# Kernel tuning notes

Hardware: AMD Instinct MI355X
Metric: run time of the kernel (lower is better)

Reference implementation:

```python
import jax, jax.numpy as jnp
import numpy as np

N, D_IN, D_H, D_OUT = 65536, 256, 256, 128
E, TOP_K = 16, 2


def setup_inputs() -> dict:
    key = jax.random.key(0)
    ks = jax.random.split(key, 16)
    s = 0.05
    inp = {
        'x': jax.random.normal(ks[0], (N, D_IN), jnp.float32),
        'W0': jax.random.normal(ks[1], (D_IN, D_H), jnp.float32) * s,
        'b0': jnp.zeros((D_H,), jnp.float32),
        'Wg1': jax.random.normal(ks[2], (D_H, E), jnp.float32) * s,
        'bg1': jnp.zeros((E,), jnp.float32),
        'We1': jax.random.normal(ks[3], (E, D_H, D_H), jnp.float32) * s,
        'be1': jnp.zeros((E, D_H), jnp.float32),
        'Wg2': jax.random.normal(ks[4], (D_H, E), jnp.float32) * s,
        'bg2': jnp.zeros((E,), jnp.float32),
        'We2': jax.random.normal(ks[5], (E, D_H, D_H), jnp.float32) * s,
        'be2': jnp.zeros((E, D_H), jnp.float32),
        'Wf': jax.random.normal(ks[6], (D_H, D_OUT), jnp.float32) * s,
        'bf': jnp.zeros((D_OUT,), jnp.float32),
    }
    return inp


def _moe_layer(h, Wg, bg, We, be):
    # naive gate: logits over experts, top-k, renormalized softmax of top-k vals
    logits = h @ Wg + bg                      # [N, E]
    gate_full = jax.nn.softmax(logits, axis=-1)  # returned 'gate' for std stat
    vals, idx = jax.lax.top_k(logits, TOP_K)  # [N, k]
    scores = jax.nn.softmax(vals, axis=-1)    # [N, k]
    # scatter top-k scores into dense combine weights [N, E]
    cw = (jax.nn.one_hot(idx, E, dtype=h.dtype) * scores[..., None]).sum(axis=1)
    # grouped GEMM expressed as masked per-expert GEMMs (E is small, fixed)
    y = jnp.zeros((h.shape[0], We.shape[-1]), h.dtype)
    for e in range(E):
        y = y + cw[:, e:e + 1] * (h @ We[e] + be[e])
    # torch.std defaults to unbiased (ddof=1)
    gate_std_mean = jnp.std(gate_full, axis=1, ddof=1).mean()
    return y, gate_std_mean


def reference(x, W0, b0, Wg1, bg1, We1, be1, Wg2, bg2, We2, be2, Wf, bf):
    h = jax.nn.relu(x @ W0 + b0)
    h, g1 = _moe_layer(h, Wg1, bg1, We1, be1)
    h = jax.nn.relu(h)
    h, g2 = _moe_layer(h, Wg2, bg2, We2, be2)
    h = jax.nn.relu(h)
    out = h @ Wf + bf
    gate_std_means_mean = (g1 + g2) * 0.5
    return out, gate_std_means_mean
```

## Files before the change

kernel.cpp:

```cpp
#include <hip/hip_runtime.h>
#include <math.h>

#define NT 65536
#define DH 256
#define DO 128
#define NE 16

struct RInfo { int e1, e2; float s1, s2; };

typedef __attribute__((ext_vector_type(8))) short bh8;
typedef __attribute__((ext_vector_type(4))) float fx4;

static __device__ __forceinline__ short f2bf(float f) {
    union { float f; unsigned u; } v; v.f = f;
    return (short)((v.u + 0x7FFFu + ((v.u >> 16) & 1u)) >> 16);
}

template<bool RELU>
__global__ __launch_bounds__(256)
void gemm_dense(const float* __restrict__ A, const float* __restrict__ B,
                const float* __restrict__ bias, float* __restrict__ C,
                int ncols)
{
    __shared__ float As[128][36];
    __shared__ float Bs[32][132];
    const int tid = threadIdx.x;
    const int tx = tid & 15, ty = tid >> 4;
    const int rowBase = blockIdx.x * 128;
    const int colBase = blockIdx.y * 128;

    float acc[8][8];
#pragma unroll
    for (int i = 0; i < 8; ++i)
#pragma unroll
        for (int j = 0; j < 8; ++j) acc[i][j] = 0.f;

    for (int kt = 0; kt < DH; kt += 32) {
        {
            const int r = tid >> 3, k4 = (tid & 7) << 2;
#pragma unroll
            for (int it = 0; it < 4; ++it) {
                const float4 v = *reinterpret_cast<const float4*>(
                    &A[(size_t)(rowBase + r + 32 * it) * DH + kt + k4]);
                *reinterpret_cast<float4*>(&As[r + 32 * it][k4]) = v;
            }
        }
        {
            const int kr = tid >> 5, c4 = (tid & 31) << 2;
#pragma unroll
            for (int it = 0; it < 4; ++it) {
                const float4 v = *reinterpret_cast<const float4*>(
                    &B[(size_t)(kt + kr + 8 * it) * ncols + colBase + c4]);
                *reinterpret_cast<float4*>(&Bs[kr + 8 * it][c4]) = v;
            }
        }
        __syncthreads();
#pragma unroll
        for (int k4 = 0; k4 < 32; k4 += 4) {
            alignas(16) float ar[8][4];
#pragma unroll
            for (int i = 0; i < 8; ++i)
                *reinterpret_cast<float4*>(ar[i]) =
                    *reinterpret_cast<const float4*>(&As[ty * 8 + i][k4]);
#pragma unroll
            for (int kk = 0; kk < 4; ++kk) {
                alignas(16) float br[8];
                *reinterpret_cast<float4*>(&br[0]) =
                    *reinterpret_cast<const float4*>(&Bs[k4 + kk][tx * 8]);
                *reinterpret_cast<float4*>(&br[4]) =
                    *reinterpret_cast<const float4*>(&Bs[k4 + kk][tx * 8 + 4]);
#pragma unroll
                for (int i = 0; i < 8; ++i) {
                    const float a = ar[i][kk];
#pragma unroll
                    for (int j = 0; j < 8; ++j)
                        acc[i][j] = fmaf(a, br[j], acc[i][j]);
                }
            }
        }
        __syncthreads();
    }
    alignas(16) float bb[8];
#pragma unroll
    for (int j = 0; j < 8; ++j) bb[j] = bias[colBase + tx * 8 + j];
#pragma unroll
    for (int i = 0; i < 8; ++i) {
        const size_t row = rowBase + ty * 8 + i;
        alignas(16) float o[8];
#pragma unroll
        for (int j = 0; j < 8; ++j) {
            float v = acc[i][j] + bb[j];
            if (RELU) v = fmaxf(v, 0.f);
            o[j] = v;
        }
        float* p = &C[row * (size_t)ncols + colBase + tx * 8];
        *reinterpret_cast<float4*>(p)     = *reinterpret_cast<float4*>(&o[0]);
        *reinterpret_cast<float4*>(p + 4) = *reinterpret_cast<float4*>(&o[4]);
    }
}

__global__ __launch_bounds__(256)
void gate_kernel(const float* __restrict__ H, const float* __restrict__ Wg,
                 const float* __restrict__ bg, RInfo* __restrict__ info,
                 float* gsum)
{
    __shared__ float wgs[256][17];
    __shared__ float hs[16][260];
    __shared__ float lg[16][17];
    __shared__ float sbg[16];
    __shared__ float sds[16];
    const int tid = threadIdx.x;
    const int rowBase = blockIdx.x * 16;

#pragma unroll
    for (int i = 0; i < 16; ++i) {
        const int idx = tid + 256 * i;
        wgs[idx >> 4][idx & 15] = Wg[idx];
    }
    if (tid < 16) sbg[tid] = bg[tid];
#pragma unroll
    for (int it = 0; it < 4; ++it) {
        const int flat = (tid + 256 * it) * 4;
        const int r = flat >> 8, k = flat & 255;
        *reinterpret_cast<float4*>(&hs[r][k]) =
            *reinterpret_cast<const float4*>(&H[(size_t)(rowBase + r) * DH + k]);
    }
    __syncthreads();
    {
        const int r = tid >> 4, e = tid & 15;
        float acc = 0.f;
#pragma unroll 8
        for (int k = 0; k < 256; ++k) acc = fmaf(hs[r][k], wgs[k][e], acc);
        lg[r][e] = acc + sbg[e];
    }
    __syncthreads();
    if (tid < 16) {
        const int row = rowBase + tid;
        float l[16];
#pragma unroll
        for (int i = 0; i < 16; ++i) l[i] = lg[tid][i];
        int i1 = 0; float v1 = l[0];
#pragma unroll
        for (int i = 1; i < 16; ++i) if (l[i] > v1) { v1 = l[i]; i1 = i; }
        int i2 = -1; float v2 = -INFINITY;
#pragma unroll
        for (int i = 0; i < 16; ++i) if (i != i1 && l[i] > v2) { v2 = l[i]; i2 = i; }
        const float t = expf(v2 - v1);
        const float s1 = 1.f / (1.f + t);
        const float s2 = t / (1.f + t);
        float p[16]; float S = 0.f;
#pragma unroll
        for (int i = 0; i < 16; ++i) { p[i] = expf(l[i] - v1); S += p[i]; }
        const float inv = 1.f / S;
        float sq = 0.f;
#pragma unroll
        for (int i = 0; i < 16; ++i) { const float q = p[i] * inv; sq = fmaf(q, q, sq); }
        const float var = (sq - 1.0f / 16.0f) * (1.0f / 15.0f);
        const float sd = sqrtf(fmaxf(var, 0.f));

        RInfo ri; ri.e1 = i1; ri.e2 = i2; ri.s1 = s1; ri.s2 = s2;
        info[row] = ri;
        sds[tid] = sd;
    }
    __syncthreads();
    if (tid == 0) {
        float s = 0.f;
#pragma unroll
        for (int i = 0; i < 16; ++i) s += sds[i];
        atomicAdd(gsum, s);
    }
}

__global__ void zero_gsum(float* gsum)
{
    if (threadIdx.x < 2) gsum[threadIdx.x] = 0.f;
}

__global__ __launch_bounds__(256)
void count_kernel(const RInfo* __restrict__ info, int* __restrict__ bc0,
                  int* __restrict__ bc1)
{
    __shared__ int h0[NE], h1[NE];
    const int tid = threadIdx.x, b = blockIdx.x;
    if (tid < NE) { h0[tid] = 0; h1[tid] = 0; }
    __syncthreads();
    const RInfo ri = info[b * 256 + tid];
    atomicAdd(&h0[ri.e1], 1);
    atomicAdd(&h1[ri.e2], 1);
    __syncthreads();
    if (tid < NE) {
        bc0[tid * 256 + b] = h0[tid];
        bc1[tid * 256 + b] = h1[tid];
    }
}

__global__ void scan2_kernel(const int* __restrict__ bc0, const int* __restrict__ bc1,
                             int* cnt0, int* cnt1, int* off0, int* off1,
                             int* __restrict__ bo0, int* __restrict__ bo1)
{
    __shared__ int tot0[NE], tot1[NE], base0[NE], base1[NE];
    const int t = threadIdx.x;
    if (t < NE) {
        int s = 0;
        for (int b = 0; b < 256; ++b) s += bc0[t * 256 + b];
        tot0[t] = s; cnt0[t] = s;
    } else if (t < 2 * NE) {
        const int e = t - NE;
        int s = 0;
        for (int b = 0; b < 256; ++b) s += bc1[e * 256 + b];
        tot1[e] = s; cnt1[e] = s;
    }
    __syncthreads();
    if (t == 0) { int a = 0; for (int e = 0; e < NE; ++e) { base0[e] = a; off0[e] = a; a += tot0[e]; } }
    if (t == 1) { int a = 0; for (int e = 0; e < NE; ++e) { base1[e] = a; off1[e] = a; a += tot1[e]; } }
    __syncthreads();
    if (t < NE) {
        int run = base0[t];
        for (int b = 0; b < 256; ++b) { bo0[t * 256 + b] = run; run += bc0[t * 256 + b]; }
    } else if (t < 2 * NE) {
        const int e = t - NE;
        int run = base1[e];
        for (int b = 0; b < 256; ++b) { bo1[e * 256 + b] = run; run += bc1[e * 256 + b]; }
    }
}

__global__ __launch_bounds__(256)
void scatter2_kernel(const RInfo* __restrict__ info, const int* __restrict__ bo0,
                     const int* __restrict__ bo1, int* __restrict__ l0,
                     int* __restrict__ l1)
{
    __shared__ int h0[NE], h1[NE];
    const int tid = threadIdx.x, b = blockIdx.x;
    if (tid < NE) { h0[tid] = 0; h1[tid] = 0; }
    __syncthreads();
    const int r = b * 256 + tid;
    const RInfo ri = info[r];
    const int p0 = atomicAdd(&h0[ri.e1], 1);
    const int p1 = atomicAdd(&h1[ri.e2], 1);
    l0[bo0[ri.e1 * 256 + b] + p0] = r;
    l1[bo1[ri.e2 * 256 + b] + p1] = r;
}

template<int SLOT>
__global__ __launch_bounds__(256)
void gemm_expert(const float* __restrict__ Hin, const float* __restrict__ We,
                 const float* __restrict__ be, const RInfo* __restrict__ info,
                 const int* __restrict__ list, const int* __restrict__ cnts,
                 const int* __restrict__ offs, float* __restrict__ P)
{
    __shared__ float As[128][36];
    __shared__ float Bs[32][132];
    __shared__ int   rs[128];
    __shared__ float ss[128];

    int c = blockIdx.x, e;
    int cnt = 0;
    for (e = 0; e < NE; ++e) {
        cnt = cnts[e];
        const int nch = (cnt + 127) >> 7;
        if (c < nch) break;
        c -= nch;
    }
    if (e >= NE) return;
    const int m = min(128, cnt - c * 128);
    const int base = offs[e] + c * 128;
    const int tid = threadIdx.x;
    const int tx = tid & 15, ty = tid >> 4;
    const int colBase = blockIdx.y * 128;

    if (tid < 128) {
        const int g = list[base + min(tid, m - 1)];
        rs[tid] = g;
        const RInfo ri = info[g];
        ss[tid] = (SLOT == 0) ? ri.s1 : ri.s2;
    }
    __syncthreads();

    const float* B = We + (size_t)e * DH * DH;

    float acc[8][8];
#pragma unroll
    for (int i = 0; i < 8; ++i)
#pragma unroll
        for (int j = 0; j < 8; ++j) acc[i][j] = 0.f;

    for (int kt = 0; kt < DH; kt += 32) {
        {
            const int r = tid >> 3, k4 = (tid & 7) << 2;
#pragma unroll
            for (int it = 0; it < 4; ++it) {
                const int g = rs[r + 32 * it];
                const float4 v = *reinterpret_cast<const float4*>(
                    &Hin[(size_t)g * DH + kt + k4]);
                *reinterpret_cast<float4*>(&As[r + 32 * it][k4]) = v;
            }
        }
        {
            const int kr = tid >> 5, c4 = (tid & 31) << 2;
#pragma unroll
            for (int it = 0; it < 4; ++it) {
                const float4 v = *reinterpret_cast<const float4*>(
                    &B[(size_t)(kt + kr + 8 * it) * DH + colBase + c4]);
                *reinterpret_cast<float4*>(&Bs[kr + 8 * it][c4]) = v;
            }
        }
        __syncthreads();
#pragma unroll
        for (int k4 = 0; k4 < 32; k4 += 4) {
            alignas(16) float ar[8][4];
#pragma unroll
            for (int i = 0; i < 8; ++i)
                *reinterpret_cast<float4*>(ar[i]) =
                    *reinterpret_cast<const float4*>(&As[ty * 8 + i][k4]);
#pragma unroll
            for (int kk = 0; kk < 4; ++kk) {
                alignas(16) float br[8];
                *reinterpret_cast<float4*>(&br[0]) =
                    *reinterpret_cast<const float4*>(&Bs[k4 + kk][tx * 8]);
                *reinterpret_cast<float4*>(&br[4]) =
                    *reinterpret_cast<const float4*>(&Bs[k4 + kk][tx * 8 + 4]);
#pragma unroll
                for (int i = 0; i < 8; ++i) {
                    const float a = ar[i][kk];
#pragma unroll
                    for (int j = 0; j < 8; ++j)
                        acc[i][j] = fmaf(a, br[j], acc[i][j]);
                }
            }
        }
        __syncthreads();
    }

    alignas(16) float bb[8];
#pragma unroll
    for (int j = 0; j < 8; ++j) bb[j] = be[(size_t)e * DH + colBase + tx * 8 + j];
#pragma unroll
    for (int i = 0; i < 8; ++i) {
        const int rl = ty * 8 + i;
        if (rl < m) {
            const int g = rs[rl];
            const float s = ss[rl];
            alignas(16) float o[8];
#pragma unroll
            for (int j = 0; j < 8; ++j) o[j] = s * (acc[i][j] + bb[j]);
            float* pp = &P[(size_t)g * DH + colBase + tx * 8];
            if (SLOT == 0) {
                *reinterpret_cast<float4*>(pp)     = *reinterpret_cast<float4*>(&o[0]);
                *reinterpret_cast<float4*>(pp + 4) = *reinterpret_cast<float4*>(&o[4]);
            } else {
                const float4 p0 = *reinterpret_cast<const float4*>(pp);
                const float4 p1 = *reinterpret_cast<const float4*>(pp + 4);
                alignas(16) float h[8];
                h[0] = fmaxf(o[0] + p0.x, 0.f); h[1] = fmaxf(o[1] + p0.y, 0.f);
                h[2] = fmaxf(o[2] + p0.z, 0.f); h[3] = fmaxf(o[3] + p0.w, 0.f);
                h[4] = fmaxf(o[4] + p1.x, 0.f); h[5] = fmaxf(o[5] + p1.y, 0.f);
                h[6] = fmaxf(o[6] + p1.z, 0.f); h[7] = fmaxf(o[7] + p1.w, 0.f);
                *reinterpret_cast<float4*>(pp)     = *reinterpret_cast<float4*>(&h[0]);
                *reinterpret_cast<float4*>(pp + 4) = *reinterpret_cast<float4*>(&h[4]);
            }
        }
    }
}

__global__ __launch_bounds__(256)
void transp_bf16(const float* __restrict__ W, short* __restrict__ WT,
                 int K, int N)
{
    __shared__ float t[32][33];
    const int k0 = blockIdx.x * 32, n0 = blockIdx.y * 32;
    const size_t off = (size_t)blockIdx.z * K * N;
    const int c = threadIdx.x & 31, r8 = threadIdx.x >> 5;
#pragma unroll
    for (int it = 0; it < 4; ++it) {
        const int r = r8 + it * 8;
        t[r][c] = W[off + (size_t)(k0 + r) * N + n0 + c];
    }
    __syncthreads();
#pragma unroll
    for (int it = 0; it < 4; ++it) {
        const int r = r8 + it * 8;
        WT[off + (size_t)(n0 + r) * K + k0 + c] = f2bf(t[c][r]);
    }
}

template<int SLOT>
__global__ __launch_bounds__(256)
void gemm_expert_bf16(const float* __restrict__ Yin, const short* __restrict__ WeT,
                      const float* __restrict__ be, const RInfo* __restrict__ info,
                      const int* __restrict__ list, const int* __restrict__ cnts,
                      const int* __restrict__ offs, float* __restrict__ P)
{
    __shared__ bh8 As8[512];
    __shared__ bh8 Bs8[512];
    __shared__ int   rs[128];
    __shared__ float ss[128];

    int c = blockIdx.x, e;
    int cnt = 0;
    for (e = 0; e < NE; ++e) {
        cnt = cnts[e];
        const int nch = (cnt + 127) >> 7;
        if (c < nch) break;
        c -= nch;
    }
    if (e >= NE) return;
    const int m = min(128, cnt - c * 128);
    const int base = offs[e] + c * 128;
    const int tid = threadIdx.x;

    if (tid < 128) {
        const int g = list[base + min(tid, m - 1)];
        rs[tid] = g;
        const RInfo ri = info[g];
        ss[tid] = (SLOT == 0) ? ri.s1 : ri.s2;
    }
    __syncthreads();

    const int colBase = blockIdx.y * 128;
    const int lane = tid & 63, wave = tid >> 6;
    const int wr = wave >> 1, wc = wave & 1;
    const short* Bw = WeT + (size_t)e * DH * DH;

    fx4 acc[4][4];
    const fx4 z = {0.f, 0.f, 0.f, 0.f};
#pragma unroll
    for (int i = 0; i < 4; ++i)
#pragma unroll
        for (int j = 0; j < 4; ++j) acc[i][j] = z;

    const int d0 = tid, d1 = tid + 256;
    const int ar0 = d0 >> 2, ak0 = d0 & 3;
    const int ar1 = d1 >> 2, ak1 = d1 & 3;
    const int g0 = ar0 * 4 + (ak0 ^ ((ar0 >> 1) & 3));
    const int g1 = ar1 * 4 + (ak1 ^ ((ar1 >> 1) & 3));
    const size_t arow0 = (size_t)rs[ar0] * DH, arow1 = (size_t)rs[ar1] * DH;
    const size_t brow0 = (size_t)(colBase + ar0) * DH, brow1 = (size_t)(colBase + ar1) * DH;

    for (int kt = 0; kt < DH; kt += 32) {
        {
            const float* s0 = &Yin[arow0 + kt + ak0 * 8];
            const float4 f0 = *reinterpret_cast<const float4*>(s0);
            const float4 f1 = *reinterpret_cast<const float4*>(s0 + 4);
            bh8 v;
            v[0]=f2bf(f0.x); v[1]=f2bf(f0.y); v[2]=f2bf(f0.z); v[3]=f2bf(f0.w);
            v[4]=f2bf(f1.x); v[5]=f2bf(f1.y); v[6]=f2bf(f1.z); v[7]=f2bf(f1.w);
            As8[g0] = v;
            const float* s1 = &Yin[arow1 + kt + ak1 * 8];
            const float4 f2 = *reinterpret_cast<const float4*>(s1);
            const float4 f3 = *reinterpret_cast<const float4*>(s1 + 4);
            bh8 w;
            w[0]=f2bf(f2.x); w[1]=f2bf(f2.y); w[2]=f2bf(f2.z); w[3]=f2bf(f2.w);
            w[4]=f2bf(f3.x); w[5]=f2bf(f3.y); w[6]=f2bf(f3.z); w[7]=f2bf(f3.w);
            As8[g1] = w;
        }
        {
            Bs8[g0] = *reinterpret_cast<const bh8*>(&Bw[brow0 + kt + ak0 * 8]);
            Bs8[g1] = *reinterpret_cast<const bh8*>(&Bw[brow1 + kt + ak1 * 8]);
        }
        __syncthreads();
        const int kq = lane >> 4, lm = lane & 15;
        bh8 af[4], bfr[4];
#pragma unroll
        for (int i = 0; i < 4; ++i) {
            const int rl = wr * 64 + i * 16 + lm;
            af[i] = As8[rl * 4 + (kq ^ ((rl >> 1) & 3))];
            const int cl = wc * 64 + i * 16 + lm;
            bfr[i] = Bs8[cl * 4 + (kq ^ ((cl >> 1) & 3))];
        }
#pragma unroll
        for (int i = 0; i < 4; ++i)
#pragma unroll
            for (int j = 0; j < 4; ++j)
                acc[i][j] = __builtin_amdgcn_mfma_f32_16x16x32_bf16(
                    af[i], bfr[j], acc[i][j], 0, 0, 0);
        __syncthreads();
    }

    const int rq = lane >> 4, lm = lane & 15;
#pragma unroll
    for (int i = 0; i < 4; ++i) {
#pragma unroll
        for (int j = 0; j < 4; ++j) {
            const int rl = wr * 64 + i * 16 + rq * 4 + j;
            if (rl < m) {
                const int g = rs[rl];
                const float s = ss[rl];
#pragma unroll
                for (int nf = 0; nf < 4; ++nf) {
                    const int cl = colBase + wc * 64 + nf * 16 + lm;
                    float* pp = &P[(size_t)g * DH + cl];
                    const float o = s * (acc[i][nf][j] + be[(size_t)e * DH + cl]);
                    if (SLOT == 0) *pp = o;
                    else           *pp = fmaxf(*pp + o, 0.f);
                }
            }
        }
    }
}

__global__ __launch_bounds__(256)
void gemm_final_bf16(const float* __restrict__ Hin, const short* __restrict__ WT,
                     const float* __restrict__ bias, float* __restrict__ C,
                     const float* gsum, float* scalar_out)
{
    __shared__ bh8 As8[512];
    __shared__ bh8 Bs8[512];
    const int tid = threadIdx.x;
    const int rowBase = blockIdx.x * 128;

    if (blockIdx.x == 0 && tid == 0)
        *scalar_out = (gsum[0] + gsum[1]) * (0.5f / (float)NT);

    const int lane = tid & 63, wave = tid >> 6;
    const int wr = wave >> 1, wc = wave & 1;

    fx4 acc[4][4];
    const fx4 z = {0.f, 0.f, 0.f, 0.f};
#pragma unroll
    for (int i = 0; i < 4; ++i)
#pragma unroll
        for (int j = 0; j < 4; ++j) acc[i][j] = z;

    const int d0 = tid, d1 = tid + 256;
    const int ar0 = d0 >> 2, ak0 = d0 & 3;
    const int ar1 = d1 >> 2, ak1 = d1 & 3;
    const int g0 = ar0 * 4 + (ak0 ^ ((ar0 >> 1) & 3));
    const int g1 = ar1 * 4 + (ak1 ^ ((ar1 >> 1) & 3));
    const size_t arow0 = (size_t)(rowBase + ar0) * DH, arow1 = (size_t)(rowBase + ar1) * DH;
    const size_t brow0 = (size_t)ar0 * DH, brow1 = (size_t)ar1 * DH;

    for (int kt = 0; kt < DH; kt += 32) {
        {
            const float* s0 = &Hin[arow0 + kt + ak0 * 8];
            const float4 f0 = *reinterpret_cast<const float4*>(s0);
            const float4 f1 = *reinterpret_cast<const float4*>(s0 + 4);
            bh8 v;
            v[0]=f2bf(f0.x); v[1]=f2bf(f0.y); v[2]=f2bf(f0.z); v[3]=f2bf(f0.w);
            v[4]=f2bf(f1.x); v[5]=f2bf(f1.y); v[6]=f2bf(f1.z); v[7]=f2bf(f1.w);
            As8[g0] = v;
            const float* s1 = &Hin[arow1 + kt + ak1 * 8];
            const float4 f2 = *reinterpret_cast<const float4*>(s1);
            const float4 f3 = *reinterpret_cast<const float4*>(s1 + 4);
            bh8 w;
            w[0]=f2bf(f2.x); w[1]=f2bf(f2.y); w[2]=f2bf(f2.z); w[3]=f2bf(f2.w);
            w[4]=f2bf(f3.x); w[5]=f2bf(f3.y); w[6]=f2bf(f3.z); w[7]=f2bf(f3.w);
            As8[g1] = w;
        }
        {
            Bs8[g0] = *reinterpret_cast<const bh8*>(&WT[brow0 + kt + ak0 * 8]);
            Bs8[g1] = *reinterpret_cast<const bh8*>(&WT[brow1 + kt + ak1 * 8]);
        }
        __syncthreads();
        const int kq = lane >> 4, lm = lane & 15;
        bh8 af[4], bfr[4];
#pragma unroll
        for (int i = 0; i < 4; ++i) {
            const int rl = wr * 64 + i * 16 + lm;
            af[i] = As8[rl * 4 + (kq ^ ((rl >> 1) & 3))];
            const int cl = wc * 64 + i * 16 + lm;
            bfr[i] = Bs8[cl * 4 + (kq ^ ((cl >> 1) & 3))];
        }
#pragma unroll
        for (int i = 0; i < 4; ++i)
#pragma unroll
            for (int j = 0; j < 4; ++j)
                acc[i][j] = __builtin_amdgcn_mfma_f32_16x16x32_bf16(
                    af[i], bfr[j], acc[i][j], 0, 0, 0);
        __syncthreads();
    }

    const int rq = lane >> 4, lm = lane & 15;
#pragma unroll
    for (int i = 0; i < 4; ++i) {
#pragma unroll
        for (int j = 0; j < 4; ++j) {
            const int rl = rowBase + wr * 64 + i * 16 + rq * 4 + j;
#pragma unroll
            for (int nf = 0; nf < 4; ++nf) {
                const int cl = wc * 64 + nf * 16 + lm;
                C[(size_t)rl * DO + cl] = acc[i][nf][j] + bias[cl];
            }
        }
    }
}

extern "C" void kernel_launch(void* const* d_in, const int* in_sizes, int n_in,
                              void* d_out, int out_size, void* d_ws, size_t ws_size,
                              hipStream_t stream)
{
    const float* x   = (const float*)d_in[0];
    const float* W0  = (const float*)d_in[1];
    const float* b0  = (const float*)d_in[2];
    const float* Wg1 = (const float*)d_in[3];
    const float* bg1 = (const float*)d_in[4];
    const float* We1 = (const float*)d_in[5];
    const float* be1 = (const float*)d_in[6];
    const float* Wg2 = (const float*)d_in[7];
    const float* bg2 = (const float*)d_in[8];
    const float* We2 = (const float*)d_in[9];
    const float* be2 = (const float*)d_in[10];
    const float* Wf  = (const float*)d_in[11];
    const float* bf  = (const float*)d_in[12];
    float* out = (float*)d_out;

    char* w = (char*)d_ws;
    float* H    = (float*)w; w += (size_t)NT * DH * 4;
    float* Y    = (float*)w; w += (size_t)NT * DH * 4;
    RInfo* info = (RInfo*)w; w += (size_t)NT * sizeof(RInfo);
    int* l0   = (int*)w; w += (size_t)NT * 4;
    int* l1   = (int*)w; w += (size_t)NT * 4;
    int* bc0  = (int*)w; w += NE * 256 * 4;
    int* bc1  = (int*)w; w += NE * 256 * 4;
    int* bo0  = (int*)w; w += NE * 256 * 4;
    int* bo1  = (int*)w; w += NE * 256 * 4;
    int* cnt0 = (int*)w; w += 64;
    int* cnt1 = (int*)w; w += 64;
    int* off0 = (int*)w; w += 64;
    int* off1 = (int*)w; w += 64;
    float* gsum = (float*)w; w += 64;
    short* WeT = (short*)w; w += (size_t)NE * DH * DH * 2;
    short* WfT = (short*)w; w += (size_t)DH * DO * 2;

    const dim3 blk(256);
    const int MAXCH = NT / 128 + NE;

    zero_gsum<<<dim3(1), dim3(64), 0, stream>>>(gsum);
    transp_bf16<<<dim3(8, 8, 16), blk, 0, stream>>>(We2, WeT, DH, DH);
    transp_bf16<<<dim3(8, 4, 1),  blk, 0, stream>>>(Wf,  WfT, DH, DO);

    gemm_dense<true><<<dim3(NT / 128, 2), blk, 0, stream>>>(x, W0, b0, H, DH);

    gate_kernel<<<dim3(NT / 16), blk, 0, stream>>>(H, Wg1, bg1, info, &gsum[0]);
    count_kernel<<<dim3(NT / 256), blk, 0, stream>>>(info, bc0, bc1);
    scan2_kernel<<<dim3(1), dim3(64), 0, stream>>>(bc0, bc1, cnt0, cnt1, off0, off1, bo0, bo1);
    scatter2_kernel<<<dim3(NT / 256), blk, 0, stream>>>(info, bo0, bo1, l0, l1);
    gemm_expert<0><<<dim3(MAXCH, 2), blk, 0, stream>>>(H, We1, be1, info, l0, cnt0, off0, Y);
    gemm_expert<1><<<dim3(MAXCH, 2), blk, 0, stream>>>(H, We1, be1, info, l1, cnt1, off1, Y);

    gate_kernel<<<dim3(NT / 16), blk, 0, stream>>>(Y, Wg2, bg2, info, &gsum[1]);
    count_kernel<<<dim3(NT / 256), blk, 0, stream>>>(info, bc0, bc1);
    scan2_kernel<<<dim3(1), dim3(64), 0, stream>>>(bc0, bc1, cnt0, cnt1, off0, off1, bo0, bo1);
    scatter2_kernel<<<dim3(NT / 256), blk, 0, stream>>>(info, bo0, bo1, l0, l1);
    gemm_expert_bf16<0><<<dim3(MAXCH, 2), blk, 0, stream>>>(Y, WeT, be2, info, l0, cnt0, off0, H);
    gemm_expert_bf16<1><<<dim3(MAXCH, 2), blk, 0, stream>>>(Y, WeT, be2, info, l1, cnt1, off1, H);

    gemm_final_bf16<<<dim3(NT / 128, 1), blk, 0, stream>>>(H, WfT, bf, out, gsum, out + (size_t)NT * DO);
}
```

Before: 614.6 us.

## Widen dense and expert GEMM tiles to cover all 256 output columns per block

```diff
diff --git a/kernel.cpp b/kernel.cpp
--- a/kernel.cpp
+++ b/kernel.cpp
@@ -17,17 +17,15 @@
 }
 
 template<bool RELU>
-__global__ __launch_bounds__(256)
+__global__ __launch_bounds__(512)
 void gemm_dense(const float* __restrict__ A, const float* __restrict__ B,
-                const float* __restrict__ bias, float* __restrict__ C,
-                int ncols)
+                const float* __restrict__ bias, float* __restrict__ C)
 {
     __shared__ float As[128][36];
-    __shared__ float Bs[32][132];
+    __shared__ float Bs[32][260];
     const int tid = threadIdx.x;
-    const int tx = tid & 15, ty = tid >> 4;
+    const int tx = tid & 31, ty = tid >> 5;
     const int rowBase = blockIdx.x * 128;
-    const int colBase = blockIdx.y * 128;
 
     float acc[8][8];
 #pragma unroll
@@ -38,19 +36,19 @@
     for (int kt = 0; kt < DH; kt += 32) {
         {
             const int r = tid >> 3, k4 = (tid & 7) << 2;
+#pragma unroll
+            for (int it = 0; it < 2; ++it) {
+                const float4 v = *reinterpret_cast<const float4*>(
+                    &A[(size_t)(rowBase + r + 64 * it) * DH + kt + k4]);
+                *reinterpret_cast<float4*>(&As[r + 64 * it][k4]) = v;
+            }
+        }
+        {
+            const int kr = tid >> 6, c4 = (tid & 63) << 2;
 #pragma unroll
             for (int it = 0; it < 4; ++it) {
                 const float4 v = *reinterpret_cast<const float4*>(
-                    &A[(size_t)(rowBase + r + 32 * it) * DH + kt + k4]);
-                *reinterpret_cast<float4*>(&As[r + 32 * it][k4]) = v;
-            }
-        }
-        {
-            const int kr = tid >> 5, c4 = (tid & 31) << 2;
-#pragma unroll
-            for (int it = 0; it < 4; ++it) {
-                const float4 v = *reinterpret_cast<const float4*>(
-                    &B[(size_t)(kt + kr + 8 * it) * ncols + colBase + c4]);
+                    &B[(size_t)(kt + kr + 8 * it) * DH + c4]);
                 *reinterpret_cast<float4*>(&Bs[kr + 8 * it][c4]) = v;
             }
         }
@@ -82,7 +80,7 @@
     }
     alignas(16) float bb[8];
 #pragma unroll
-    for (int j = 0; j < 8; ++j) bb[j] = bias[colBase + tx * 8 + j];
+    for (int j = 0; j < 8; ++j) bb[j] = bias[tx * 8 + j];
 #pragma unroll
     for (int i = 0; i < 8; ++i) {
         const size_t row = rowBase + ty * 8 + i;
@@ -93,7 +91,7 @@
             if (RELU) v = fmaxf(v, 0.f);
             o[j] = v;
         }
-        float* p = &C[row * (size_t)ncols + colBase + tx * 8];
+        float* p = &C[row * (size_t)DH + tx * 8];
         *reinterpret_cast<float4*>(p)     = *reinterpret_cast<float4*>(&o[0]);
         *reinterpret_cast<float4*>(p + 4) = *reinterpret_cast<float4*>(&o[4]);
     }
@@ -242,14 +240,14 @@
 }
 
 template<int SLOT>
-__global__ __launch_bounds__(256)
+__global__ __launch_bounds__(512)
 void gemm_expert(const float* __restrict__ Hin, const float* __restrict__ We,
                  const float* __restrict__ be, const RInfo* __restrict__ info,
                  const int* __restrict__ list, const int* __restrict__ cnts,
                  const int* __restrict__ offs, float* __restrict__ P)
 {
     __shared__ float As[128][36];
-    __shared__ float Bs[32][132];
+    __shared__ float Bs[32][260];
     __shared__ int   rs[128];
     __shared__ float ss[128];
 
@@ -265,8 +263,7 @@
     const int m = min(128, cnt - c * 128);
     const int base = offs[e] + c * 128;
     const int tid = threadIdx.x;
-    const int tx = tid & 15, ty = tid >> 4;
-    const int colBase = blockIdx.y * 128;
+    const int tx = tid & 31, ty = tid >> 5;
 
     if (tid < 128) {
         const int g = list[base + min(tid, m - 1)];
@@ -288,19 +285,19 @@
         {
             const int r = tid >> 3, k4 = (tid & 7) << 2;
 #pragma unroll
-            for (int it = 0; it < 4; ++it) {
-                const int g = rs[r + 32 * it];
+            for (int it = 0; it < 2; ++it) {
+                const int g = rs[r + 64 * it];
                 const float4 v = *reinterpret_cast<const float4*>(
                     &Hin[(size_t)g * DH + kt + k4]);
-                *reinterpret_cast<float4*>(&As[r + 32 * it][k4]) = v;
-            }
-        }
-        {
-            const int kr = tid >> 5, c4 = (tid & 31) << 2;
+                *reinterpret_cast<float4*>(&As[r + 64 * it][k4]) = v;
+            }
+        }
+        {
+            const int kr = tid >> 6, c4 = (tid & 63) << 2;
 #pragma unroll
             for (int it = 0; it < 4; ++it) {
                 const float4 v = *reinterpret_cast<const float4*>(
-                    &B[(size_t)(kt + kr + 8 * it) * DH + colBase + c4]);
+                    &B[(size_t)(kt + kr + 8 * it) * DH + c4]);
                 *reinterpret_cast<float4*>(&Bs[kr + 8 * it][c4]) = v;
             }
         }
@@ -333,7 +330,7 @@
 
     alignas(16) float bb[8];
 #pragma unroll
-    for (int j = 0; j < 8; ++j) bb[j] = be[(size_t)e * DH + colBase + tx * 8 + j];
+    for (int j = 0; j < 8; ++j) bb[j] = be[(size_t)e * DH + tx * 8 + j];
 #pragma unroll
     for (int i = 0; i < 8; ++i) {
         const int rl = ty * 8 + i;
@@ -343,7 +340,7 @@
             alignas(16) float o[8];
 #pragma unroll
             for (int j = 0; j < 8; ++j) o[j] = s * (acc[i][j] + bb[j]);
-            float* pp = &P[(size_t)g * DH + colBase + tx * 8];
+            float* pp = &P[(size_t)g * DH + tx * 8];
             if (SLOT == 0) {
                 *reinterpret_cast<float4*>(pp)     = *reinterpret_cast<float4*>(&o[0]);
                 *reinterpret_cast<float4*>(pp + 4) = *reinterpret_cast<float4*>(&o[4]);
@@ -384,14 +381,14 @@
 }
 
 template<int SLOT>
-__global__ __launch_bounds__(256)
+__global__ __launch_bounds__(512)
 void gemm_expert_bf16(const float* __restrict__ Yin, const short* __restrict__ WeT,
                       const float* __restrict__ be, const RInfo* __restrict__ info,
                       const int* __restrict__ list, const int* __restrict__ cnts,
                       const int* __restrict__ offs, float* __restrict__ P)
 {
     __shared__ bh8 As8[512];
-    __shared__ bh8 Bs8[512];
+    __shared__ bh8 Bs8[1024];
     __shared__ int   rs[128];
     __shared__ float ss[128];
 
@@ -416,9 +413,8 @@
     }
     __syncthreads();
 
-    const int colBase = blockIdx.y * 128;
     const int lane = tid & 63, wave = tid >> 6;
-    const int wr = wave >> 1, wc = wave & 1;
+    const int wr = wave >> 2, wc = wave & 3;
     const short* Bw = WeT + (size_t)e * DH * DH;
 
     fx4 acc[4][4];
@@ -428,34 +424,28 @@
 #pragma unroll
         for (int j = 0; j < 4; ++j) acc[i][j] = z;
 
-    const int d0 = tid, d1 = tid + 256;
-    const int ar0 = d0 >> 2, ak0 = d0 & 3;
-    const int ar1 = d1 >> 2, ak1 = d1 & 3;
-    const int g0 = ar0 * 4 + (ak0 ^ ((ar0 >> 1) & 3));
-    const int g1 = ar1 * 4 + (ak1 ^ ((ar1 >> 1) & 3));
-    const size_t arow0 = (size_t)rs[ar0] * DH, arow1 = (size_t)rs[ar1] * DH;
-    const size_t brow0 = (size_t)(colBase + ar0) * DH, brow1 = (size_t)(colBase + ar1) * DH;
+    const int ar0 = tid >> 2, ak0 = tid & 3;
+    const int ga  = ar0 * 4 + (ak0 ^ ((ar0 >> 1) & 3));
+    const int bcol0 = tid >> 2, bk0 = tid & 3;
+    const int gb0 = bcol0 * 4 + (bk0 ^ ((bcol0 >> 1) & 3));
+    const int bcol1 = (tid + 512) >> 2, bk1 = tid & 3;
+    const int gb1 = bcol1 * 4 + (bk1 ^ ((bcol1 >> 1) & 3));
+    const size_t arow = (size_t)rs[ar0] * DH;
+    const size_t brow0 = (size_t)bcol0 * DH, brow1 = (size_t)bcol1 * DH;
 
     for (int kt = 0; kt < DH; kt += 32) {
         {
-            const float* s0 = &Yin[arow0 + kt + ak0 * 8];
+            const float* s0 = &Yin[arow + kt + ak0 * 8];
             const float4 f0 = *reinterpret_cast<const float4*>(s0);
             const float4 f1 = *reinterpret_cast<const float4*>(s0 + 4);
             bh8 v;
             v[0]=f2bf(f0.x); v[1]=f2bf(f0.y); v[2]=f2bf(f0.z); v[3]=f2bf(f0.w);
             v[4]=f2bf(f1.x); v[5]=f2bf(f1.y); v[6]=f2bf(f1.z); v[7]=f2bf(f1.w);
-            As8[g0] = v;
-            const float* s1 = &Yin[arow1 + kt + ak1 * 8];
-            const float4 f2 = *reinterpret_cast<const float4*>(s1);
-            const float4 f3 = *reinterpret_cast<const float4*>(s1 + 4);
-            bh8 w;
-            w[0]=f2bf(f2.x); w[1]=f2bf(f2.y); w[2]=f2bf(f2.z); w[3]=f2bf(f2.w);
-            w[4]=f2bf(f3.x); w[5]=f2bf(f3.y); w[6]=f2bf(f3.z); w[7]=f2bf(f3.w);
-            As8[g1] = w;
-        }
-        {
-            Bs8[g0] = *reinterpret_cast<const bh8*>(&Bw[brow0 + kt + ak0 * 8]);
-            Bs8[g1] = *reinterpret_cast<const bh8*>(&Bw[brow1 + kt + ak1 * 8]);
+            As8[ga] = v;
+        }
+        {
+            Bs8[gb0] = *reinterpret_cast<const bh8*>(&Bw[brow0 + kt + bk0 * 8]);
+            Bs8[gb1] = *reinterpret_cast<const bh8*>(&Bw[brow1 + kt + bk1 * 8]);
         }
         __syncthreads();
         const int kq = lane >> 4, lm = lane & 15;
@@ -487,7 +477,7 @@
                 const float s = ss[rl];
 #pragma unroll
                 for (int nf = 0; nf < 4; ++nf) {
-                    const int cl = colBase + wc * 64 + nf * 16 + lm;
+                    const int cl = wc * 64 + nf * 16 + lm;
                     float* pp = &P[(size_t)g * DH + cl];
                     const float o = s * (acc[i][nf][j] + be[(size_t)e * DH + cl]);
                     if (SLOT == 0) *pp = o;
@@ -621,28 +611,27 @@
     short* WeT = (short*)w; w += (size_t)NE * DH * DH * 2;
     short* WfT = (short*)w; w += (size_t)DH * DO * 2;
 
-    const dim3 blk(256);
     const int MAXCH = NT / 128 + NE;
 
     zero_gsum<<<dim3(1), dim3(64), 0, stream>>>(gsum);
-    transp_bf16<<<dim3(8, 8, 16), blk, 0, stream>>>(We2, WeT, DH, DH);
-    transp_bf16<<<dim3(8, 4, 1),  blk, 0, stream>>>(Wf,  WfT, DH, DO);
-
-    gemm_dense<true><<<dim3(NT / 128, 2), blk, 0, stream>>>(x, W0, b0, H, DH);
-
-    gate_kernel<<<dim3(NT / 16), blk, 0, stream>>>(H, Wg1, bg1, info, &gsum[0]);
-    count_kernel<<<dim3(NT / 256), blk, 0, stream>>>(info, bc0, bc1);
+    transp_bf16<<<dim3(8, 8, 16), dim3(256), 0, stream>>>(We2, WeT, DH, DH);
+    transp_bf16<<<dim3(8, 4, 1),  dim3(256), 0, stream>>>(Wf,  WfT, DH, DO);
+
+    gemm_dense<true><<<dim3(NT / 128), dim3(512), 0, stream>>>(x, W0, b0, H);
+
+    gate_kernel<<<dim3(NT / 16), dim3(256), 0, stream>>>(H, Wg1, bg1, info, &gsum[0]);
+    count_kernel<<<dim3(NT / 256), dim3(256), 0, stream>>>(info, bc0, bc1);
     scan2_kernel<<<dim3(1), dim3(64), 0, stream>>>(bc0, bc1, cnt0, cnt1, off0, off1, bo0, bo1);
-    scatter2_kernel<<<dim3(NT / 256), blk, 0, stream>>>(info, bo0, bo1, l0, l1);
-    gemm_expert<0><<<dim3(MAXCH, 2), blk, 0, stream>>>(H, We1, be1, info, l0, cnt0, off0, Y);
-    gemm_expert<1><<<dim3(MAXCH, 2), blk, 0, stream>>>(H, We1, be1, info, l1, cnt1, off1, Y);
-
-    gate_kernel<<<dim3(NT / 16), blk, 0, stream>>>(Y, Wg2, bg2, info, &gsum[1]);
-    count_kernel<<<dim3(NT / 256), blk, 0, stream>>>(info, bc0, bc1);
+    scatter2_kernel<<<dim3(NT / 256), dim3(256), 0, stream>>>(info, bo0, bo1, l0, l1);
+    gemm_expert<0><<<dim3(MAXCH), dim3(512), 0, stream>>>(H, We1, be1, info, l0, cnt0, off0, Y);
+    gemm_expert<1><<<dim3(MAXCH), dim3(512), 0, stream>>>(H, We1, be1, info, l1, cnt1, off1, Y);
+
+    gate_kernel<<<dim3(NT / 16), dim3(256), 0, stream>>>(Y, Wg2, bg2, info, &gsum[1]);
+    count_kernel<<<dim3(NT / 256), dim3(256), 0, stream>>>(info, bc0, bc1);
     scan2_kernel<<<dim3(1), dim3(64), 0, stream>>>(bc0, bc1, cnt0, cnt1, off0, off1, bo0, bo1);
-    scatter2_kernel<<<dim3(NT / 256), blk, 0, stream>>>(info, bo0, bo1, l0, l1);
-    gemm_expert_bf16<0><<<dim3(MAXCH, 2), blk, 0, stream>>>(Y, WeT, be2, info, l0, cnt0, off0, H);
-    gemm_expert_bf16<1><<<dim3(MAXCH, 2), blk, 0, stream>>>(Y, WeT, be2, info, l1, cnt1, off1, H);
-
-    gemm_final_bf16<<<dim3(NT / 128, 1), blk, 0, stream>>>(H, WfT, bf, out, gsum, out + (size_t)NT * DO);
-}
+    scatter2_kernel<<<dim3(NT / 256), dim3(256), 0, stream>>>(info, bo0, bo1, l0, l1);
+    gemm_expert_bf16<0><<<dim3(MAXCH), dim3(512), 0, stream>>>(Y, WeT, be2, info, l0, cnt0, off0, H);
+    gemm_expert_bf16<1><<<dim3(MAXCH), dim3(512), 0, stream>>>(Y, WeT, be2, info, l1, cnt1, off1, H);
+
+    gemm_final_bf16<<<dim3(NT / 128), dim3(256), 0, stream>>>(H, WfT, bf, out, gsum, out + (size_t)NT * DO);
+}
```

Result: slower. 709.2 us (+15.4%).

## Emit bf16 activation copies for later bf16 GEMMs and halve fp32 K-tile

Applied to the files above, without the earlier changes.

```diff
diff --git a/kernel.cpp b/kernel.cpp
--- a/kernel.cpp
+++ b/kernel.cpp
@@ -22,41 +22,34 @@
                 const float* __restrict__ bias, float* __restrict__ C,
                 int ncols)
 {
-    __shared__ float As[128][36];
-    __shared__ float Bs[32][132];
+    __shared__ float As[128][24];
+    __shared__ float Bs[16][132];
     const int tid = threadIdx.x;
     const int tx = tid & 15, ty = tid >> 4;
     const int rowBase = blockIdx.x * 128;
     const int colBase = blockIdx.y * 128;
 
+    const int ra0 = tid >> 2, ga = tid & 3;
+    const int kb0 = tid >> 5, cb = tid & 31;
+
     float acc[8][8];
 #pragma unroll
     for (int i = 0; i < 8; ++i)
 #pragma unroll
         for (int j = 0; j < 8; ++j) acc[i][j] = 0.f;
 
-    for (int kt = 0; kt < DH; kt += 32) {
-        {
-            const int r = tid >> 3, k4 = (tid & 7) << 2;
-#pragma unroll
-            for (int it = 0; it < 4; ++it) {
-                const float4 v = *reinterpret_cast<const float4*>(
-                    &A[(size_t)(rowBase + r + 32 * it) * DH + kt + k4]);
-                *reinterpret_cast<float4*>(&As[r + 32 * it][k4]) = v;
-            }
-        }
-        {
-            const int kr = tid >> 5, c4 = (tid & 31) << 2;
-#pragma unroll
-            for (int it = 0; it < 4; ++it) {
-                const float4 v = *reinterpret_cast<const float4*>(
-                    &B[(size_t)(kt + kr + 8 * it) * ncols + colBase + c4]);
-                *reinterpret_cast<float4*>(&Bs[kr + 8 * it][c4]) = v;
-            }
-        }
-        __syncthreads();
-#pragma unroll
-        for (int k4 = 0; k4 < 32; k4 += 4) {
+    for (int kt = 0; kt < DH; kt += 16) {
+        *reinterpret_cast<float4*>(&As[ra0][ga * 4]) =
+            *reinterpret_cast<const float4*>(&A[(size_t)(rowBase + ra0) * DH + kt + ga * 4]);
+        *reinterpret_cast<float4*>(&As[ra0 + 64][ga * 4]) =
+            *reinterpret_cast<const float4*>(&A[(size_t)(rowBase + ra0 + 64) * DH + kt + ga * 4]);
+        *reinterpret_cast<float4*>(&Bs[kb0][cb * 4]) =
+            *reinterpret_cast<const float4*>(&B[(size_t)(kt + kb0) * ncols + colBase + cb * 4]);
+        *reinterpret_cast<float4*>(&Bs[kb0 + 8][cb * 4]) =
+            *reinterpret_cast<const float4*>(&B[(size_t)(kt + kb0 + 8) * ncols + colBase + cb * 4]);
+        __syncthreads();
+#pragma unroll
+        for (int k4 = 0; k4 < 16; k4 += 4) {
             alignas(16) float ar[8][4];
 #pragma unroll
             for (int i = 0; i < 8; ++i)
@@ -246,10 +239,11 @@
 void gemm_expert(const float* __restrict__ Hin, const float* __restrict__ We,
                  const float* __restrict__ be, const RInfo* __restrict__ info,
                  const int* __restrict__ list, const int* __restrict__ cnts,
-                 const int* __restrict__ offs, float* __restrict__ P)
-{
-    __shared__ float As[128][36];
-    __shared__ float Bs[32][132];
+                 const int* __restrict__ offs, float* __restrict__ P,
+                 short* __restrict__ Ybf)
+{
+    __shared__ float As[128][24];
+    __shared__ float Bs[16][132];
     __shared__ int   rs[128];
     __shared__ float ss[128];
 
@@ -277,6 +271,10 @@
     __syncthreads();
 
     const float* B = We + (size_t)e * DH * DH;
+    const int ra0 = tid >> 2, ga = tid & 3;
+    const int kb0 = tid >> 5, cb = tid & 31;
+    const size_t arow0 = (size_t)rs[ra0] * DH;
+    const size_t arow1 = (size_t)rs[ra0 + 64] * DH;
 
     float acc[8][8];
 #pragma unroll
@@ -284,29 +282,18 @@
 #pragma unroll
         for (int j = 0; j < 8; ++j) acc[i][j] = 0.f;
 
-    for (int kt = 0; kt < DH; kt += 32) {
-        {
-            const int r = tid >> 3, k4 = (tid & 7) << 2;
-#pragma unroll
-            for (int it = 0; it < 4; ++it) {
-                const int g = rs[r + 32 * it];
-                const float4 v = *reinterpret_cast<const float4*>(
-                    &Hin[(size_t)g * DH + kt + k4]);
-                *reinterpret_cast<float4*>(&As[r + 32 * it][k4]) = v;
-            }
-        }
-        {
-            const int kr = tid >> 5, c4 = (tid & 31) << 2;
-#pragma unroll
-            for (int it = 0; it < 4; ++it) {
-                const float4 v = *reinterpret_cast<const float4*>(
-                    &B[(size_t)(kt + kr + 8 * it) * DH + colBase + c4]);
-                *reinterpret_cast<float4*>(&Bs[kr + 8 * it][c4]) = v;
-            }
-        }
-        __syncthreads();
-#pragma unroll
-        for (int k4 = 0; k4 < 32; k4 += 4) {
+    for (int kt = 0; kt < DH; kt += 16) {
+        *reinterpret_cast<float4*>(&As[ra0][ga * 4]) =
+            *reinterpret_cast<const float4*>(&Hin[arow0 + kt + ga * 4]);
+        *reinterpret_cast<float4*>(&As[ra0 + 64][ga * 4]) =
+            *reinterpret_cast<const float4*>(&Hin[arow1 + kt + ga * 4]);
+        *reinterpret_cast<float4*>(&Bs[kb0][cb * 4]) =
+            *reinterpret_cast<const float4*>(&B[(size_t)(kt + kb0) * DH + colBase + cb * 4]);
+        *reinterpret_cast<float4*>(&Bs[kb0 + 8][cb * 4]) =
+            *reinterpret_cast<const float4*>(&B[(size_t)(kt + kb0 + 8) * DH + colBase + cb * 4]);
+        __syncthreads();
+#pragma unroll
+        for (int k4 = 0; k4 < 16; k4 += 4) {
             alignas(16) float ar[8][4];
 #pragma unroll
             for (int i = 0; i < 8; ++i)
@@ -357,6 +344,12 @@
                 h[6] = fmaxf(o[6] + p1.z, 0.f); h[7] = fmaxf(o[7] + p1.w, 0.f);
                 *reinterpret_cast<float4*>(pp)     = *reinterpret_cast<float4*>(&h[0]);
                 *reinterpret_cast<float4*>(pp + 4) = *reinterpret_cast<float4*>(&h[4]);
+                if (Ybf) {
+                    bh8 yb;
+#pragma unroll
+                    for (int j = 0; j < 8; ++j) yb[j] = f2bf(h[j]);
+                    *reinterpret_cast<bh8*>(&Ybf[(size_t)g * DH + colBase + tx * 8]) = yb;
+                }
             }
         }
     }
@@ -383,12 +376,14 @@
     }
 }
 
-template<int SLOT>
-__global__ __launch_bounds__(256)
-void gemm_expert_bf16(const float* __restrict__ Yin, const short* __restrict__ WeT,
+template<int SLOT, int BFA>
+__global__ __launch_bounds__(256)
+void gemm_expert_bf16(const float* __restrict__ Yf, const short* __restrict__ Abf,
+                      const short* __restrict__ WeT,
                       const float* __restrict__ be, const RInfo* __restrict__ info,
                       const int* __restrict__ list, const int* __restrict__ cnts,
-                      const int* __restrict__ offs, float* __restrict__ P)
+                      const int* __restrict__ offs, float* __restrict__ P,
+                      short* __restrict__ Hbf)
 {
     __shared__ bh8 As8[512];
     __shared__ bh8 Bs8[512];
@@ -437,15 +432,18 @@
     const size_t brow0 = (size_t)(colBase + ar0) * DH, brow1 = (size_t)(colBase + ar1) * DH;
 
     for (int kt = 0; kt < DH; kt += 32) {
-        {
-            const float* s0 = &Yin[arow0 + kt + ak0 * 8];
+        if (BFA) {
+            As8[g0] = *reinterpret_cast<const bh8*>(&Abf[arow0 + kt + ak0 * 8]);
+            As8[g1] = *reinterpret_cast<const bh8*>(&Abf[arow1 + kt + ak1 * 8]);
+        } else {
+            const float* s0 = &Yf[arow0 + kt + ak0 * 8];
             const float4 f0 = *reinterpret_cast<const float4*>(s0);
             const float4 f1 = *reinterpret_cast<const float4*>(s0 + 4);
             bh8 v;
             v[0]=f2bf(f0.x); v[1]=f2bf(f0.y); v[2]=f2bf(f0.z); v[3]=f2bf(f0.w);
             v[4]=f2bf(f1.x); v[5]=f2bf(f1.y); v[6]=f2bf(f1.z); v[7]=f2bf(f1.w);
             As8[g0] = v;
-            const float* s1 = &Yin[arow1 + kt + ak1 * 8];
+            const float* s1 = &Yf[arow1 + kt + ak1 * 8];
             const float4 f2 = *reinterpret_cast<const float4*>(s1);
             const float4 f3 = *reinterpret_cast<const float4*>(s1 + 4);
             bh8 w;
@@ -490,16 +488,23 @@
                     const int cl = colBase + wc * 64 + nf * 16 + lm;
                     float* pp = &P[(size_t)g * DH + cl];
                     const float o = s * (acc[i][nf][j] + be[(size_t)e * DH + cl]);
-                    if (SLOT == 0) *pp = o;
-                    else           *pp = fmaxf(*pp + o, 0.f);
+                    if (SLOT == 0) {
+                        *pp = o;
+                    } else {
+                        const float v = fmaxf(*pp + o, 0.f);
+                        if (BFA) Hbf[(size_t)g * DH + cl] = f2bf(v);
+                        else     *pp = v;
+                    }
                 }
             }
         }
     }
 }
 
-__global__ __launch_bounds__(256)
-void gemm_final_bf16(const float* __restrict__ Hin, const short* __restrict__ WT,
+template<int BFA>
+__global__ __launch_bounds__(256)
+void gemm_final_bf16(const float* __restrict__ Hf, const short* __restrict__ Habf,
+                     const short* __restrict__ WT,
                      const float* __restrict__ bias, float* __restrict__ C,
                      const float* gsum, float* scalar_out)
 {
@@ -530,15 +535,18 @@
     const size_t brow0 = (size_t)ar0 * DH, brow1 = (size_t)ar1 * DH;
 
     for (int kt = 0; kt < DH; kt += 32) {
-        {
-            const float* s0 = &Hin[arow0 + kt + ak0 * 8];
+        if (BFA) {
+            As8[g0] = *reinterpret_cast<const bh8*>(&Habf[arow0 + kt + ak0 * 8]);
+            As8[g1] = *reinterpret_cast<const bh8*>(&Habf[arow1 + kt + ak1 * 8]);
+        } else {
+            const float* s0 = &Hf[arow0 + kt + ak0 * 8];
             const float4 f0 = *reinterpret_cast<const float4*>(s0);
             const float4 f1 = *reinterpret_cast<const float4*>(s0 + 4);
             bh8 v;
             v[0]=f2bf(f0.x); v[1]=f2bf(f0.y); v[2]=f2bf(f0.z); v[3]=f2bf(f0.w);
             v[4]=f2bf(f1.x); v[5]=f2bf(f1.y); v[6]=f2bf(f1.z); v[7]=f2bf(f1.w);
             As8[g0] = v;
-            const float* s1 = &Hin[arow1 + kt + ak1 * 8];
+            const float* s1 = &Hf[arow1 + kt + ak1 * 8];
             const float4 f2 = *reinterpret_cast<const float4*>(s1);
             const float4 f3 = *reinterpret_cast<const float4*>(s1 + 4);
             bh8 w;
@@ -620,29 +628,37 @@
     float* gsum = (float*)w; w += 64;
     short* WeT = (short*)w; w += (size_t)NE * DH * DH * 2;
     short* WfT = (short*)w; w += (size_t)DH * DO * 2;
-
-    const dim3 blk(256);
+    short* Ybf = (short*)w; w += (size_t)NT * DH * 2;
+    const bool roomy = (size_t)(w - (char*)d_ws) <= ws_size;
+    short* Hbf = (short*)Y;
+
     const int MAXCH = NT / 128 + NE;
 
     zero_gsum<<<dim3(1), dim3(64), 0, stream>>>(gsum);
-    transp_bf16<<<dim3(8, 8, 16), blk, 0, stream>>>(We2, WeT, DH, DH);
-    transp_bf16<<<dim3(8, 4, 1),  blk, 0, stream>>>(Wf,  WfT, DH, DO);
-
-    gemm_dense<true><<<dim3(NT / 128, 2), blk, 0, stream>>>(x, W0, b0, H, DH);
-
-    gate_kernel<<<dim3(NT / 16), blk, 0, stream>>>(H, Wg1, bg1, info, &gsum[0]);
-    count_kernel<<<dim3(NT / 256), blk, 0, stream>>>(info, bc0, bc1);
+    transp_bf16<<<dim3(8, 8, 16), dim3(256), 0, stream>>>(We2, WeT, DH, DH);
+    transp_bf16<<<dim3(8, 4, 1),  dim3(256), 0, stream>>>(Wf,  WfT, DH, DO);
+
+    gemm_dense<true><<<dim3(NT / 128, 2), dim3(256), 0, stream>>>(x, W0, b0, H, DH);
+
+    gate_kernel<<<dim3(NT / 16), dim3(256), 0, stream>>>(H, Wg1, bg1, info, &gsum[0]);
+    count_kernel<<<dim3(NT / 256), dim3(256), 0, stream>>>(info, bc0, bc1);
     scan2_kernel<<<dim3(1), dim3(64), 0, stream>>>(bc0, bc1, cnt0, cnt1, off0, off1, bo0, bo1);
-    scatter2_kernel<<<dim3(NT / 256), blk, 0, stream>>>(info, bo0, bo1, l0, l1);
-    gemm_expert<0><<<dim3(MAXCH, 2), blk, 0, stream>>>(H, We1, be1, info, l0, cnt0, off0, Y);
-    gemm_expert<1><<<dim3(MAXCH, 2), blk, 0, stream>>>(H, We1, be1, info, l1, cnt1, off1, Y);
-
-    gate_kernel<<<dim3(NT / 16), blk, 0, stream>>>(Y, Wg2, bg2, info, &gsum[1]);
-    count_kernel<<<dim3(NT / 256), blk, 0, stream>>>(info, bc0, bc1);
+    scatter2_kernel<<<dim3(NT / 256), dim3(256), 0, stream>>>(info, bo0, bo1, l0, l1);
+    gemm_expert<0><<<dim3(MAXCH, 2), dim3(256), 0, stream>>>(H, We1, be1, info, l0, cnt0, off0, Y, nullptr);
+    gemm_expert<1><<<dim3(MAXCH, 2), dim3(256), 0, stream>>>(H, We1, be1, info, l1, cnt1, off1, Y,
+                                                             roomy ? Ybf : nullptr);
+
+    gate_kernel<<<dim3(NT / 16), dim3(256), 0, stream>>>(Y, Wg2, bg2, info, &gsum[1]);
+    count_kernel<<<dim3(NT / 256), dim3(256), 0, stream>>>(info, bc0, bc1);
     scan2_kernel<<<dim3(1), dim3(64), 0, stream>>>(bc0, bc1, cnt0, cnt1, off0, off1, bo0, bo1);
-    scatter2_kernel<<<dim3(NT / 256), blk, 0, stream>>>(info, bo0, bo1, l0, l1);
-    gemm_expert_bf16<0><<<dim3(MAXCH, 2), blk, 0, stream>>>(Y, WeT, be2, info, l0, cnt0, off0, H);
-    gemm_expert_bf16<1><<<dim3(MAXCH, 2), blk, 0, stream>>>(Y, WeT, be2, info, l1, cnt1, off1, H);
-
-    gemm_final_bf16<<<dim3(NT / 128, 1), blk, 0, stream>>>(H, WfT, bf, out, gsum, out + (size_t)NT * DO);
-}
+    scatter2_kernel<<<dim3(NT / 256), dim3(256), 0, stream>>>(info, bo0, bo1, l0, l1);
+    if (roomy) {
+        gemm_expert_bf16<0,1><<<dim3(MAXCH, 2), dim3(256), 0, stream>>>(Y, Ybf, WeT, be2, info, l0, cnt0, off0, H, nullptr);
+        gemm_expert_bf16<1,1><<<dim3(MAXCH, 2), dim3(256), 0, stream>>>(Y, Ybf, WeT, be2, info, l1, cnt1, off1, H, Hbf);
+        gemm_final_bf16<1><<<dim3(NT / 128), dim3(256), 0, stream>>>(H, Hbf, WfT, bf, out, gsum, out + (size_t)NT * DO);
+    } else {
+        gemm_expert_bf16<0,0><<<dim3(MAXCH, 2), dim3(256), 0, stream>>>(Y, nullptr, WeT, be2, info, l0, cnt0, off0, H, nullptr);
+        gemm_expert_bf16<1,0><<<dim3(MAXCH, 2), dim3(256), 0, stream>>>(Y, nullptr, WeT, be2, info, l1, cnt1, off1, H, nullptr);
+        gemm_final_bf16<0><<<dim3(NT / 128), dim3(256), 0, stream>>>(H, nullptr, WfT, bf, out, gsum, out + (size_t)NT * DO);
+    }
+}
```

After: 630.0 us. 2.5% more time.
